# Performance work log

Hardware: AMD Instinct MI355X
Metric: run time of the kernel (lower is better)

Reference implementation:

```python
import jax, jax.numpy as jnp
import numpy as np

T_MAX = 20  # max_seq_length


def setup_inputs() -> dict:
    key = jax.random.key(0)
    ks = jax.random.split(key, 24)
    B, H, A, V, Tc = 64, 512, 512, 50257, 19
    s = 0.02
    inp = {}
    inp["features"] = jax.random.normal(ks[0], (B, H), jnp.float32)
    inp["captions"] = jax.random.randint(ks[1], (B, Tc), 0, V)
    lens = jax.random.randint(ks[2], (B, 1), 1, T_MAX + 1)
    inp["lengths"] = -jnp.sort(-lens, axis=0)  # descending so sort_ind is identity
    inp["embed_table"] = jax.random.uniform(ks[3], (V, H), jnp.float32, -0.1, 0.1)
    # LSTM cell (PyTorch layout): input = [emb; attended] -> 2H
    inp["W_ih"] = jax.random.normal(ks[4], (4 * H, 2 * H), jnp.float32) * s
    inp["W_hh"] = jax.random.normal(ks[5], (4 * H, H), jnp.float32) * s
    inp["b_ih"] = jnp.zeros((4 * H,), jnp.float32)
    inp["b_hh"] = jnp.zeros((4 * H,), jnp.float32)
    # attention
    inp["W_enc"] = jax.random.normal(ks[6], (H, A), jnp.float32) * s
    inp["b_enc"] = jnp.zeros((A,), jnp.float32)
    inp["W_dec"] = jax.random.normal(ks[7], (H, A), jnp.float32) * s
    inp["b_dec"] = jnp.zeros((A,), jnp.float32)
    inp["W_full"] = jax.random.normal(ks[8], (A, 1), jnp.float32) * s
    inp["b_full"] = jnp.zeros((1,), jnp.float32)
    # init_h / init_c / f_beta / fc
    inp["W_hinit"] = jax.random.normal(ks[9], (H, H), jnp.float32) * s
    inp["b_hinit"] = jnp.zeros((H,), jnp.float32)
    inp["W_cinit"] = jax.random.normal(ks[10], (H, H), jnp.float32) * s
    inp["b_cinit"] = jnp.zeros((H,), jnp.float32)
    inp["W_beta"] = jax.random.normal(ks[11], (H, H), jnp.float32) * s
    inp["b_beta"] = jnp.zeros((H,), jnp.float32)
    inp["W_fc"] = jax.random.uniform(ks[12], (H, V), jnp.float32, -0.1, 0.1)
    inp["b_fc"] = jnp.zeros((V,), jnp.float32)
    return inp


def _decode(features, embed_table, W_ih, W_hh, b_ih, b_hh, W_enc, b_enc,
            W_dec, b_dec, W_full, b_full, W_hinit, b_hinit, W_cinit, b_cinit,
            W_beta, b_beta, W_fc, b_fc, captions, lengths):
    B, H = features.shape
    emb = embed_table[captions]                               # (B, T-1, H)
    embeddings = jnp.concatenate([features[:, None, :], emb], axis=1)  # (B, T, H)
    encoder_out = features[:, None, :]                        # (B, 1, H) num_pixels=1
    mean_enc = encoder_out.mean(axis=1)
    h0 = mean_enc @ W_hinit + b_hinit
    c0 = mean_enc @ W_cinit + b_cinit
    att1 = encoder_out @ W_enc + b_enc                        # (B, 1, A), time-invariant
    lens = lengths[:, 0]

    def step(carry, xs):
        h, c = carry
        emb_t, t = xs
        # attention
        att2 = h @ W_dec + b_dec                              # (B, A)
        e = jax.nn.relu(att1 + att2[:, None, :]) @ W_full + b_full  # (B, 1, 1)
        alpha = jax.nn.softmax(e[..., 0], axis=1)             # (B, 1)
        awe = (encoder_out * alpha[..., None]).sum(axis=1)    # (B, H)
        gate = jax.nn.sigmoid(h @ W_beta + b_beta)
        awe = gate * awe
        # LSTM cell (PyTorch gate order i, f, g, o)
        x = jnp.concatenate([emb_t, awe], axis=1)             # (B, 2H)
        gates = x @ W_ih.T + b_ih + h @ W_hh.T + b_hh
        i, f, g, o = jnp.split(gates, 4, axis=1)
        c_new = jax.nn.sigmoid(f) * c + jax.nn.sigmoid(i) * jnp.tanh(g)
        h_new = jax.nn.sigmoid(o) * jnp.tanh(c_new)
        preds = h_new @ W_fc + b_fc                           # (B, V)
        mask = (t < lens)[:, None]
        h = jnp.where(mask, h_new, h)
        c = jnp.where(mask, c_new, c)
        out_t = jnp.where(mask, preds, jnp.zeros_like(preds))
        return (h, c), out_t

    xs = (embeddings.transpose(1, 0, 2), jnp.arange(T_MAX))
    _, outs = jax.lax.scan(step, (h0, c0), xs)                # (T, B, V)
    return outs.transpose(1, 0, 2)                            # (B, T, V)


def reference(features, captions, lengths, embed_table, W_ih, W_hh, b_ih, b_hh,
              W_enc, b_enc, W_dec, b_dec, W_full, b_full, W_hinit, b_hinit,
              W_cinit, b_cinit, W_beta, b_beta, W_fc, b_fc):
    return _decode(features, embed_table, W_ih, W_hh, b_ih, b_hh, W_enc, b_enc,
                   W_dec, b_dec, W_full, b_full, W_hinit, b_hinit, W_cinit,
                   b_cinit, W_beta, b_beta, W_fc, b_fc, captions, lengths)
```

## Files before the change

kernel.cpp:

```cpp
#include <hip/hip_runtime.h>
#include <hip/hip_bf16.h>


#define VV 50257
#define VP 50304
#define TT 20
#define NWRK 32
#define NTILES 6288
#define NNT 393
#define NGJOBS (TT*NNT)

typedef __attribute__((ext_vector_type(4))) float f32x4;
typedef __attribute__((ext_vector_type(8))) short bf16x8;

#define MFMA(a,b,c) __builtin_amdgcn_mfma_f32_16x16x32_bf16((a),(b),(c),0,0,0)

__device__ __forceinline__ unsigned short f2bf(float f){
  union { float f; unsigned int u; } v; v.f = f;
  unsigned int u = v.u;
  return (unsigned short)((u + 0x7FFFu + ((u >> 16) & 1u)) >> 16);
}
__device__ __forceinline__ float sigf(float x){ return 1.f/(1.f + expf(-x)); }

__device__ __forceinline__ void gload_lds16(const unsigned short* g, unsigned short* l){
  __builtin_amdgcn_global_load_lds(
      (const __attribute__((address_space(1))) unsigned int*)g,
      (__attribute__((address_space(3))) unsigned int*)l, 16, 0, 0);
}

__device__ __forceinline__ void l2_load16(bf16x8* d, const unsigned short* p){
  asm volatile("global_load_dwordx4 %0, %1, off sc0" : "=v"(*d) : "v"(p));
}
__device__ __forceinline__ void l2_store2(unsigned short* p, unsigned short v){
  asm volatile("global_store_short %0, %1, off sc0" :: "v"(p), "v"(v) : "memory");
}
__device__ __forceinline__ void llc_store2(unsigned short* p, unsigned short v){
  asm volatile("global_store_short %0, %1, off sc0 sc1" :: "v"(p), "v"(v) : "memory");
}
__device__ __forceinline__ unsigned int llc_load_u32(const unsigned int* p){
  unsigned int r;
  asm volatile("global_load_dword %0, %1, off sc0 sc1\n\ts_waitcnt vmcnt(0)"
               : "=v"(r) : "v"(p) : "memory");
  return r;
}

__device__ __forceinline__ void gbar(unsigned int* flags, int widx, unsigned target){
  asm volatile("s_waitcnt vmcnt(0)" ::: "memory");
  __syncthreads();
  if(threadIdx.x == 0){
    asm volatile("global_store_dword %0, %1, off sc0 sc1"
                 :: "v"(flags + widx), "v"(target) : "memory");
  }
  if(threadIdx.x < 64){
    const unsigned int* p = flags + (threadIdx.x & 31);
    for(;;){
      unsigned v = llc_load_u32(p);
      if(__all((int)(v >= target))) break;
      __builtin_amdgcn_s_sleep(1);
    }
  }
  __syncthreads();
}

__global__ __launch_bounds__(256) void prep(const float* __restrict__ Wih,
    const float* __restrict__ Whh, unsigned short* __restrict__ Wcomb,
    unsigned short* __restrict__ We,
    const float* __restrict__ Wbeta, unsigned short* __restrict__ Wbt,
    const float* __restrict__ feat, const float* __restrict__ emb,
    const int* __restrict__ cap, unsigned short* __restrict__ EmbMat,
    const float* __restrict__ Whi, const float* __restrict__ bhi,
    const float* __restrict__ Wci, const float* __restrict__ bci,
    unsigned short* __restrict__ xbuf, float* __restrict__ cbuf){
  __shared__ float tile[64][65];
  const int blk = blockIdx.x, tid = threadIdx.x;
  if(blk < 2048){
    int j = blk;
    for(int q=0;q<4;q++){ int k = tid + 256*q;
      float v = (k < 512) ? Whh[j*512 + k] : Wih[j*1024 + k];
      Wcomb[(size_t)j*1024 + k] = f2bf(v); }
    for(int q=0;q<2;q++){ int k = tid + 256*q;
      We[(size_t)j*512 + k] = f2bf(Wih[j*1024 + k]); }
  } else if(blk < 2112){
    int tb = blk - 2048;
    int c0 = (tb & 7)*64, r0 = (tb >> 3)*64;
    int tx = tid & 63, ty = tid >> 6;
    for(int i=0;i<16;i++){
      int r = ty + i*4;
      tile[r][tx] = Wbeta[(size_t)(r0+r)*512 + c0 + tx];
    }
    __syncthreads();
    for(int i=0;i<16;i++){
      int cl = ty + i*4;
      Wbt[(size_t)(c0+cl)*512 + r0 + tx] = f2bf(tile[tx][cl]);
    }
  } else if(blk < 3392){
    int m = blk - 2112; int t = m >> 6, b = m & 63;
    const float* src = (t == 0) ? (feat + b*512) : (emb + (size_t)cap[b*19 + (t-1)]*512);
    for(int q=0;q<2;q++){ int k = tid + 256*q;
      EmbMat[(size_t)m*512 + k] = f2bf(src[k]); }
  } else {
    int b = blk - 3392;
    float ah0 = bhi[tid], ah1 = bhi[tid+256];
    float ac0 = bci[tid], ac1 = bci[tid+256];
    for(int k=0;k<512;k++){
      float f = feat[b*512 + k];
      ah0 += f * Whi[k*512 + tid];     ah1 += f * Whi[k*512 + tid + 256];
      ac0 += f * Wci[k*512 + tid];     ac1 += f * Wci[k*512 + tid + 256];
    }
    xbuf[b*512 + tid] = f2bf(ah0);  xbuf[b*512 + tid + 256] = f2bf(ah1);
    cbuf[b*512 + tid] = ac0;        cbuf[b*512 + tid + 256] = ac1;
  }
}

__global__ __launch_bounds__(256) void gemmE(const unsigned short* __restrict__ Abf,
    const unsigned short* __restrict__ Bbf, const float* __restrict__ bias1,
    const float* __restrict__ bias2, float* __restrict__ Cout, int MT){
  __shared__ __align__(16) unsigned short As[128*64];
  __shared__ __align__(16) unsigned short Bs[128*64];
  const int nwg = gridDim.x;
  const int id = blockIdx.x;
  const int q = nwg >> 3, rr = nwg & 7;
  const int xcd = id & 7, pos = id >> 3;
  const int work = (xcd < rr) ? (xcd*(q+1) + pos) : (rr*(q+1) + (xcd-rr)*q + pos);
  const int m0 = (work % MT) * 128;
  const int n0 = (work / MT) * 128;
  const int tid = threadIdx.x, lane = tid & 63, w = tid >> 6;
  const int wr = w >> 1, wc = w & 1;
  const int lrow = lane >> 3, lcol = (lane & 7) * 8;
  const int l15 = lane & 15, lhi = lane >> 4;

  f32x4 acc[4][4];
#pragma unroll
  for(int i=0;i<4;i++)
#pragma unroll
    for(int j=0;j<4;j++) acc[i][j] = f32x4{0.f,0.f,0.f,0.f};

  for(int k0=0;k0<512;k0+=64){
    __syncthreads();
#pragma unroll
    for(int i=0;i<4;i++){
      int c = w*4 + i;
      int row = c*8 + lrow;
      gload_lds16(Abf + (size_t)(m0+row)*512 + k0 + lcol, As + c*512);
      gload_lds16(Bbf + (size_t)(n0+row)*512 + k0 + lcol, Bs + c*512);
    }
    asm volatile("s_waitcnt vmcnt(0)" ::: "memory");
    __syncthreads();
#pragma unroll
    for(int kk=0;kk<64;kk+=32){
      bf16x8 af[4], bfv[4];
#pragma unroll
      for(int mf=0;mf<4;mf++)
        af[mf] = *(const bf16x8*)(As + (wr*64 + mf*16 + l15)*64 + kk + lhi*8);
#pragma unroll
      for(int nf=0;nf<4;nf++)
        bfv[nf] = *(const bf16x8*)(Bs + (wc*64 + nf*16 + l15)*64 + kk + lhi*8);
#pragma unroll
      for(int mf=0;mf<4;mf++)
#pragma unroll
        for(int nf=0;nf<4;nf++)
          acc[mf][nf] = MFMA(af[mf], bfv[nf], acc[mf][nf]);
    }
  }
#pragma unroll
  for(int mf=0;mf<4;mf++)
#pragma unroll
    for(int nf=0;nf<4;nf++){
      int n = n0 + wc*64 + nf*16 + l15;
#pragma unroll
      for(int r=0;r<4;r++){
        int m = m0 + wr*64 + mf*16 + lhi*4 + r;
        int gate = n >> 9, col = n & 511;
        Cout[((size_t)m*512 + col)*4 + gate] = acc[mf][nf][r] + bias1[n] + bias2[n];
      }
    }
}

__global__ __launch_bounds__(256) void recur(
    const unsigned short* __restrict__ Wcomb,
    const unsigned short* __restrict__ Wbt,
    const float* __restrict__ bbeta,
    const float* __restrict__ feat,
    const float* __restrict__ E4,
    const float* __restrict__ c0,
    const int* __restrict__ lens,
    unsigned short* xbuf,
    unsigned short* awbuf,
    unsigned short* hs,
    unsigned int* ctrs,
    const float* __restrict__ Wfc, unsigned short* Wfct,
    const float* __restrict__ bfc, float* __restrict__ out){
  extern __shared__ char LDS[];
  int* lsh = (int*)LDS;
  const int tid = threadIdx.x;

  if(tid == 0){
    unsigned xcc = 99;
    asm volatile("s_getreg_b32 %0, hwreg(HW_REG_XCC_ID)" : "=s"(xcc));
    unsigned my = 0xffffffffu;
    if(xcc == 0) my = atomicAdd(&ctrs[0], 1u);
    lsh[0] = (my < NWRK) ? 1 : 0;
    lsh[1] = (int)my;
  }
  __syncthreads();
  const int iswork = lsh[0];
  const int widx = lsh[1];
  unsigned int* flags = &ctrs[32];
  __syncthreads();

  if(!iswork){
    const int lane = tid & 63, w = tid >> 6;
    const int lrow = lane >> 3, lcol = (lane & 7)*8;
    const int l15 = lane & 15, lhi = lane >> 4;
    unsigned short* As = (unsigned short*)LDS;
    unsigned short* Bs = (unsigned short*)(LDS + 8192);
    float* et = (float*)LDS;
    float (*tile)[65] = (float(*)[65])LDS;
    int* tk = (int*)(LDS + 147440);
    bool tdone = false;

    for(;;){
      __syncthreads();
      if(tid == 0) *tk = (int)atomicAdd(&ctrs[1], 1u);
      __syncthreads();
      int j = *tk;
      __syncthreads();
      if(j >= NTILES + NGJOBS) return;

      if(j < NTILES){
        int c0t = (j % 786)*64, r0 = (j / 786)*64;
        int tx = tid & 63, ty = tid >> 6;
        for(int i=0;i<16;i++){
          int r = ty + i*4; int sc = c0t + tx;
          tile[r][tx] = (sc < VV) ? Wfc[(size_t)(r0+r)*VV + sc] : 0.f;
        }
        __syncthreads();
        for(int i=0;i<16;i++){
          int cl = ty + i*4;
          llc_store2(Wfct + (size_t)(c0t+cl)*512 + r0 + tx, f2bf(tile[tx][cl]));
        }
        asm volatile("s_waitcnt vmcnt(0)" ::: "memory");
        __syncthreads();
        if(tid == 0) atomicAdd(&ctrs[2], 1u);
        continue;
      }

      int g = j - NTILES;
      int t = g / NNT, nt = g % NNT;
      int n0 = nt * 128;
      if(!tdone){
        if(tid == 0){
          while(llc_load_u32(&ctrs[2]) < NTILES) __builtin_amdgcn_s_sleep(8);
        }
        __syncthreads();
        tdone = true;
      }
      if(tid < 64){
        const unsigned int* p = flags + (tid & 31);
        unsigned tgt = (unsigned)(2*t + 2);
        for(;;){
          unsigned v = llc_load_u32(p);
          if(__all((int)(v >= tgt))) break;
          __builtin_amdgcn_s_sleep(4);
        }
      }
      __syncthreads();

      f32x4 acc[4][2];
#pragma unroll
      for(int i=0;i<4;i++){ acc[i][0] = f32x4{0.f,0.f,0.f,0.f};
                            acc[i][1] = f32x4{0.f,0.f,0.f,0.f}; }
      for(int k0=0;k0<512;k0+=64){
        __syncthreads();
        if(w < 2){
#pragma unroll
          for(int i=0;i<4;i++){
            int c = w*4 + i; int row = c*8 + lrow;
            gload_lds16(hs + (size_t)(t*64 + row)*512 + k0 + lcol, As + c*512);
          }
        }
#pragma unroll
        for(int i=0;i<4;i++){
          int c = w*4 + i; int row = c*8 + lrow;
          gload_lds16(Wfct + (size_t)(n0 + row)*512 + k0 + lcol, Bs + c*512);
        }
        asm volatile("s_waitcnt vmcnt(0)" ::: "memory");
        __syncthreads();
#pragma unroll
        for(int kk=0;kk<64;kk+=32){
          bf16x8 af[4], bv[2];
#pragma unroll
          for(int mf=0;mf<4;mf++)
            af[mf] = *(const bf16x8*)(As + (mf*16 + l15)*64 + kk + lhi*8);
#pragma unroll
          for(int nf=0;nf<2;nf++)
            bv[nf] = *(const bf16x8*)(Bs + (w*32 + nf*16 + l15)*64 + kk + lhi*8);
#pragma unroll
          for(int mf=0;mf<4;mf++){
            acc[mf][0] = MFMA(af[mf], bv[0], acc[mf][0]);
            acc[mf][1] = MFMA(af[mf], bv[1], acc[mf][1]);
          }
        }
      }
      __syncthreads();
      float bias[2];
#pragma unroll
      for(int nf=0;nf<2;nf++){
        int n = n0 + w*32 + nf*16 + l15;
        bias[nf] = (n < VV) ? bfc[n] : 0.f;
      }
#pragma unroll
      for(int mf=0;mf<4;mf++){
#pragma unroll
        for(int r=0;r<4;r++){
          int row = mf*16 + lhi*4 + r;
          bool valid = t < lens[row];
#pragma unroll
          for(int nf=0;nf<2;nf++){
            float v = valid ? (acc[mf][nf][r] + bias[nf]) : 0.f;
            et[row*128 + w*32 + nf*16 + l15] = v;
          }
        }
      }
      __syncthreads();
      const bool edge = (n0 + 128 > VV);
#pragma unroll
      for(int qq=0;qq<8;qq++){
        int idx = tid + 256*qq;
        int row = idx >> 5, c4 = idx & 31;
        const float* er = et + row*128;
        size_t bdw = (size_t)(row*20 + t)*VV + n0;
        if(!edge){
          int al = (int)((4 - (bdw & 3)) & 3);
          int chunks = (128 - al) >> 2;
          int tail = (128 - al) & 3;
          if(c4 < chunks){
            int s0 = al + c4*4;
            f32x4 v; v[0]=er[s0]; v[1]=er[s0+1]; v[2]=er[s0+2]; v[3]=er[s0+3];
            *(f32x4*)(out + bdw + s0) = v;
          }
          if(c4 < al) out[bdw + c4] = er[c4];
          if(c4 < tail){ int s1 = al + chunks*4 + c4; out[bdw + s1] = er[s1]; }
        } else {
#pragma unroll
          for(int i=0;i<4;i++){
            int cg = n0 + c4*4 + i;
            if(cg < VV) out[bdw + (c4*4 + i)] = er[c4*4 + i];
          }
        }
      }
    }
  }

  char* WCb = LDS;
  char* WBb = LDS + 131072;
  const int lane = tid & 63, w = tid >> 6;
  const int l15 = lane & 15, lhi = lane >> 4;
  const int jj0 = widx * 16;
  const int jj = jj0 + l15;
  const int arow = w*16 + l15;

  for(int cid = tid; cid < 8192; cid += 256){
    int gr = cid >> 7, cc = cid & 127;
    size_t gg = (size_t)(gr >> 4)*512 + jj0 + (gr & 15);
    bf16x8 v = *(const bf16x8*)(Wcomb + gg*1024 + cc*8);
    *(bf16x8*)(WCb + gr*2048 + ((cc*16) ^ ((gr & 7) << 4))) = v;
  }
  for(int cid = tid; cid < 1024; cid += 256){
    int r = cid >> 6, cc = cid & 63;
    bf16x8 v = *(const bf16x8*)(Wbt + (size_t)(jj0 + r)*512 + cc*8);
    *(bf16x8*)(WBb + r*1024 + ((cc*16) ^ ((r & 7) << 4))) = v;
  }

  float c_reg[4], fe[4]; int ln[4]; unsigned short hold[4];
#pragma unroll
  for(int r=0;r<4;r++){
    int b = w*16 + lhi*4 + r;
    c_reg[r] = c0[b*512 + jj];
    fe[r]    = feat[b*512 + jj];
    ln[r]    = lens[b];
    hold[r]  = xbuf[b*512 + jj];
  }
  const float bb = bbeta[jj];
  const unsigned short* pAx = xbuf  + (size_t)arow*512 + lhi*8;
  const unsigned short* pAw = awbuf + (size_t)arow*512 + lhi*8;
  __syncthreads();

  for(int t=0;t<TT;t++){
    bf16x8 a[16];
#pragma unroll
    for(int i=0;i<16;i++) l2_load16(&a[i], pAx + i*32);
    asm volatile("s_waitcnt vmcnt(0)" ::: "memory");
    __builtin_amdgcn_sched_barrier(0);

    f32x4 acca = f32x4{0.f,0.f,0.f,0.f};
    f32x4 accg[4];
#pragma unroll
    for(int i=0;i<4;i++) accg[i] = f32x4{0.f,0.f,0.f,0.f};
#pragma unroll
    for(int i=0;i<16;i++){
      int kb2 = i*64 + lhi*16;
      bf16x8 wb = *(const bf16x8*)(WBb + l15*1024 + (kb2 ^ ((l15 & 7) << 4)));
      acca = MFMA(a[i], wb, acca);
#pragma unroll
      for(int nf=0; nf<4; nf++){
        int gr = nf*16 + l15;
        bf16x8 wg = *(const bf16x8*)(WCb + gr*2048 + (kb2 ^ ((gr & 7) << 4)));
        accg[nf] = MFMA(a[i], wg, accg[nf]);
      }
    }
#pragma unroll
    for(int r=0;r<4;r++){
      int b = w*16 + lhi*4 + r;
      float g = sigf(acca[r] + bb);
      l2_store2(awbuf + b*512 + jj, f2bf(g * fe[r]));
    }
    gbar(flags, widx, (unsigned)(2*t+1));

    f32x4 e4v[4];
#pragma unroll
    for(int r=0;r<4;r++){
      int b = w*16 + lhi*4 + r;
      e4v[r] = *(const f32x4*)(E4 + (((size_t)(t*64 + b))*512 + jj)*4);
    }
#pragma unroll
    for(int i=0;i<16;i++) l2_load16(&a[i], pAw + i*32);
    asm volatile("s_waitcnt vmcnt(0)" ::: "memory");
    __builtin_amdgcn_sched_barrier(0);
#pragma unroll
    for(int i=0;i<16;i++){
      int kb2 = 1024 + i*64 + lhi*16;
#pragma unroll
      for(int nf=0; nf<4; nf++){
        int gr = nf*16 + l15;
        bf16x8 wg = *(const bf16x8*)(WCb + gr*2048 + (kb2 ^ ((gr & 7) << 4)));
        accg[nf] = MFMA(a[i], wg, accg[nf]);
      }
    }

#pragma unroll
    for(int r=0;r<4;r++){
      int b = w*16 + lhi*4 + r;
      float iv = sigf(accg[0][r] + e4v[r][0]);
      float fv = sigf(accg[1][r] + e4v[r][1]);
      float gv = tanhf(accg[2][r] + e4v[r][2]);
      float ov = sigf(accg[3][r] + e4v[r][3]);
      float cn = fv*c_reg[r] + iv*gv;
      float hn = ov * tanhf(cn);
      bool valid = t < ln[r];
      if(valid) c_reg[r] = cn;
      unsigned short hb = valid ? f2bf(hn) : hold[r];
      hold[r] = hb;
      llc_store2(hs + (size_t)(t*64 + b)*512 + jj, hb);
      l2_store2(xbuf + b*512 + jj, hb);
    }
    gbar(flags, widx, (unsigned)(2*t+2));
  }
}

extern "C" void kernel_launch(void* const* d_in, const int* in_sizes, int n_in,
                              void* d_out, int out_size, void* d_ws, size_t ws_size,
                              hipStream_t stream){
  const float* feat  = (const float*)d_in[0];
  const int*   cap   = (const int*)  d_in[1];
  const int*   lens  = (const int*)  d_in[2];
  const float* emb   = (const float*)d_in[3];
  const float* Wih   = (const float*)d_in[4];
  const float* Whh   = (const float*)d_in[5];
  const float* bih   = (const float*)d_in[6];
  const float* bhh   = (const float*)d_in[7];
  const float* Whi   = (const float*)d_in[14];
  const float* bhi   = (const float*)d_in[15];
  const float* Wci   = (const float*)d_in[16];
  const float* bci   = (const float*)d_in[17];
  const float* Wbeta = (const float*)d_in[18];
  const float* bbeta = (const float*)d_in[19];
  const float* Wfc   = (const float*)d_in[20];
  const float* bfc   = (const float*)d_in[21];
  float* out = (float*)d_out;

  char* ws = (char*)d_ws;
  size_t off = 0;
  auto alloc = [&](size_t bytes)->void*{
    void* p = ws + off; off += (bytes + 1023) & ~(size_t)1023; return p; };
  unsigned short* Wcomb  = (unsigned short*)alloc((size_t)2048*1024*2);
  unsigned short* We     = (unsigned short*)alloc((size_t)2048*512*2);
  unsigned short* Wbt    = (unsigned short*)alloc((size_t)512*512*2);
  unsigned short* Wfct   = (unsigned short*)alloc((size_t)VP*512*2);
  unsigned short* EmbMat = (unsigned short*)alloc((size_t)1280*512*2);
  float*          E4     = (float*)alloc((size_t)1280*2048*4);
  unsigned short* xbuf   = (unsigned short*)alloc((size_t)64*512*2);
  unsigned short* awbuf  = (unsigned short*)alloc((size_t)64*512*2);
  float*          cbuf   = (float*)alloc((size_t)64*512*4);
  unsigned short* hs     = (unsigned short*)alloc((size_t)1280*512*2);
  unsigned int*   ctrs   = (unsigned int*)alloc(256);

  static_cast<void>(hipFuncSetAttribute((const void*)recur,
      hipFuncAttributeMaxDynamicSharedMemorySize, 147456));

  hipMemsetAsync(ctrs, 0, 256, stream);

  prep<<<3456, 256, 0, stream>>>(Wih, Whh, Wcomb, We, Wbeta, Wbt, feat, emb,
                                 cap, EmbMat, Whi, bhi, Wci, bci, xbuf, cbuf);

  gemmE<<<160, 256, 0, stream>>>(EmbMat, We, bih, bhh, E4, 10);

  recur<<<256, 256, 147456, stream>>>(Wcomb, Wbt, bbeta, feat, E4, cbuf, lens,
                                      xbuf, awbuf, hs, ctrs, Wfc, Wfct, bfc, out);
}
```

Measured before the change: 660.5 us.

## Keep vocab weight tile resident in LDS across all timesteps in output GEMM

```diff
diff --git a/kernel.cpp b/kernel.cpp
--- a/kernel.cpp
+++ b/kernel.cpp
@@ -8,7 +8,6 @@
 #define NWRK 32
 #define NTILES 6288
 #define NNT 393
-#define NGJOBS (TT*NNT)
 
 typedef __attribute__((ext_vector_type(4))) float f32x4;
 typedef __attribute__((ext_vector_type(8))) short bf16x8;
@@ -28,33 +27,34 @@
       (__attribute__((address_space(3))) unsigned int*)l, 16, 0, 0);
 }
 
-__device__ __forceinline__ void l2_load16(bf16x8* d, const unsigned short* p){
-  asm volatile("global_load_dwordx4 %0, %1, off sc0" : "=v"(*d) : "v"(p));
-}
-__device__ __forceinline__ void l2_store2(unsigned short* p, unsigned short v){
-  asm volatile("global_store_short %0, %1, off sc0" :: "v"(p), "v"(v) : "memory");
-}
-__device__ __forceinline__ void llc_store2(unsigned short* p, unsigned short v){
+__device__ __forceinline__ void co_load16(bf16x8* d, const unsigned short* p){
+  asm volatile("global_load_dwordx4 %0, %1, off sc0 sc1" : "=v"(*d) : "v"(p));
+}
+__device__ __forceinline__ void co_store2(unsigned short* p, unsigned short v){
   asm volatile("global_store_short %0, %1, off sc0 sc1" :: "v"(p), "v"(v) : "memory");
 }
-__device__ __forceinline__ unsigned int llc_load_u32(const unsigned int* p){
+__device__ __forceinline__ unsigned int co_load_u32(const unsigned int* p){
   unsigned int r;
   asm volatile("global_load_dword %0, %1, off sc0 sc1\n\ts_waitcnt vmcnt(0)"
                : "=v"(r) : "v"(p) : "memory");
   return r;
 }
-
-__device__ __forceinline__ void gbar(unsigned int* flags, int widx, unsigned target){
+__device__ __forceinline__ void co_store_u32(unsigned int* p, unsigned int v){
+  asm volatile("global_store_dword %0, %1, off sc0 sc1" :: "v"(p), "v"(v) : "memory");
+}
+
+__device__ __forceinline__ void gbar(unsigned int* wflags, unsigned int* pflags,
+                                     int widx, unsigned target){
   asm volatile("s_waitcnt vmcnt(0)" ::: "memory");
   __syncthreads();
   if(threadIdx.x == 0){
-    asm volatile("global_store_dword %0, %1, off sc0 sc1"
-                 :: "v"(flags + widx), "v"(target) : "memory");
+    co_store_u32(pflags + widx, target);
+    co_store_u32(wflags + widx, target);
   }
   if(threadIdx.x < 64){
-    const unsigned int* p = flags + (threadIdx.x & 31);
+    const unsigned int* p = wflags + (threadIdx.x & 31);
     for(;;){
-      unsigned v = llc_load_u32(p);
+      unsigned v = co_load_u32(p);
       if(__all((int)(v >= target))) break;
       __builtin_amdgcn_s_sleep(1);
     }
@@ -205,19 +205,22 @@
   __syncthreads();
   const int iswork = lsh[0];
   const int widx = lsh[1];
-  unsigned int* flags = &ctrs[32];
+  unsigned int* wflags = &ctrs[32];
+  unsigned int* pflags = &ctrs[64];
   __syncthreads();
 
   if(!iswork){
     const int lane = tid & 63, w = tid >> 6;
-    const int lrow = lane >> 3, lcol = (lane & 7)*8;
     const int l15 = lane & 15, lhi = lane >> 4;
-    unsigned short* As = (unsigned short*)LDS;
-    unsigned short* Bs = (unsigned short*)(LDS + 8192);
-    float* et = (float*)LDS;
+    unsigned short* Bs = (unsigned short*)LDS;
+    float* et = (float*)(LDS + 131072);
     float (*tile)[65] = (float(*)[65])LDS;
-    int* tk = (int*)(LDS + 147440);
+    int* tk = (int*)(LDS + 147456);
     bool tdone = false;
+
+    int lnv[4];
+#pragma unroll
+    for(int r=0;r<4;r++) lnv[r] = lens[w*16 + lhi*4 + r];
 
     for(;;){
       __syncthreads();
@@ -225,7 +228,7 @@
       __syncthreads();
       int j = *tk;
       __syncthreads();
-      if(j >= NTILES + NGJOBS) return;
+      if(j >= NTILES + NNT) return;
 
       if(j < NTILES){
         int c0t = (j % 786)*64, r0 = (j / 786)*64;
@@ -237,7 +240,7 @@
         __syncthreads();
         for(int i=0;i<16;i++){
           int cl = ty + i*4;
-          llc_store2(Wfct + (size_t)(c0t+cl)*512 + r0 + tx, f2bf(tile[tx][cl]));
+          co_store2(Wfct + (size_t)(c0t+cl)*512 + r0 + tx, f2bf(tile[tx][cl]));
         }
         asm volatile("s_waitcnt vmcnt(0)" ::: "memory");
         __syncthreads();
@@ -245,107 +248,100 @@
         continue;
       }
 
-      int g = j - NTILES;
-      int t = g / NNT, nt = g % NNT;
-      int n0 = nt * 128;
       if(!tdone){
         if(tid == 0){
-          while(llc_load_u32(&ctrs[2]) < NTILES) __builtin_amdgcn_s_sleep(8);
+          while(co_load_u32(&ctrs[2]) < NTILES) __builtin_amdgcn_s_sleep(16);
         }
         __syncthreads();
         tdone = true;
       }
-      if(tid < 64){
-        const unsigned int* p = flags + (tid & 31);
-        unsigned tgt = (unsigned)(2*t + 2);
-        for(;;){
-          unsigned v = llc_load_u32(p);
-          if(__all((int)(v >= tgt))) break;
-          __builtin_amdgcn_s_sleep(4);
-        }
+      const int nt = j - NTILES;
+      const int n0 = nt * 128;
+#pragma unroll
+      for(int i=0;i<32;i++){
+        int cid = tid + 256*i;
+        int row = cid >> 6, cc = cid & 63;
+        bf16x8 v = *(const bf16x8*)(Wfct + (size_t)(n0 + row)*512 + cc*8);
+        *(bf16x8*)((char*)Bs + row*1024 + ((cc*16) ^ ((row & 7) << 4))) = v;
+      }
+      float bias[8];
+#pragma unroll
+      for(int nf=0;nf<8;nf++){
+        int n = n0 + nf*16 + l15;
+        bias[nf] = (n < VV) ? bfc[n] : 0.f;
       }
       __syncthreads();
-
-      f32x4 acc[4][2];
-#pragma unroll
-      for(int i=0;i<4;i++){ acc[i][0] = f32x4{0.f,0.f,0.f,0.f};
-                            acc[i][1] = f32x4{0.f,0.f,0.f,0.f}; }
-      for(int k0=0;k0<512;k0+=64){
-        __syncthreads();
-        if(w < 2){
-#pragma unroll
-          for(int i=0;i<4;i++){
-            int c = w*4 + i; int row = c*8 + lrow;
-            gload_lds16(hs + (size_t)(t*64 + row)*512 + k0 + lcol, As + c*512);
+      const bool edge = (n0 + 128 > VV);
+
+      for(int t=0;t<TT;t++){
+        if(tid < 64){
+          const unsigned int* p = pflags + (tid & 31);
+          unsigned tgt = (unsigned)(2*t + 2);
+          for(;;){
+            unsigned v = co_load_u32(p);
+            if(__all((int)(v >= tgt))) break;
+            __builtin_amdgcn_s_sleep(8);
           }
         }
-#pragma unroll
-        for(int i=0;i<4;i++){
-          int c = w*4 + i; int row = c*8 + lrow;
-          gload_lds16(Wfct + (size_t)(n0 + row)*512 + k0 + lcol, Bs + c*512);
-        }
+        __syncthreads();
+        bf16x8 af[16];
+        const unsigned short* pA = hs + (size_t)(t*64 + w*16 + l15)*512 + lhi*8;
+#pragma unroll
+        for(int i=0;i<16;i++) co_load16(&af[i], pA + i*32);
         asm volatile("s_waitcnt vmcnt(0)" ::: "memory");
-        __syncthreads();
-#pragma unroll
-        for(int kk=0;kk<64;kk+=32){
-          bf16x8 af[4], bv[2];
-#pragma unroll
-          for(int mf=0;mf<4;mf++)
-            af[mf] = *(const bf16x8*)(As + (mf*16 + l15)*64 + kk + lhi*8);
-#pragma unroll
-          for(int nf=0;nf<2;nf++)
-            bv[nf] = *(const bf16x8*)(Bs + (w*32 + nf*16 + l15)*64 + kk + lhi*8);
-#pragma unroll
-          for(int mf=0;mf<4;mf++){
-            acc[mf][0] = MFMA(af[mf], bv[0], acc[mf][0]);
-            acc[mf][1] = MFMA(af[mf], bv[1], acc[mf][1]);
+        __builtin_amdgcn_sched_barrier(0);
+        f32x4 acc[8];
+#pragma unroll
+        for(int nf=0;nf<8;nf++) acc[nf] = f32x4{0.f,0.f,0.f,0.f};
+#pragma unroll
+        for(int i=0;i<16;i++){
+          int kb2 = i*64 + lhi*16;
+#pragma unroll
+          for(int nf=0;nf<8;nf++){
+            int gr = nf*16 + l15;
+            bf16x8 bv = *(const bf16x8*)((char*)Bs + gr*1024 + (kb2 ^ ((gr & 7) << 4)));
+            acc[nf] = MFMA(af[i], bv, acc[nf]);
           }
         }
-      }
-      __syncthreads();
-      float bias[2];
-#pragma unroll
-      for(int nf=0;nf<2;nf++){
-        int n = n0 + w*32 + nf*16 + l15;
-        bias[nf] = (n < VV) ? bfc[n] : 0.f;
-      }
-#pragma unroll
-      for(int mf=0;mf<4;mf++){
-#pragma unroll
-        for(int r=0;r<4;r++){
-          int row = mf*16 + lhi*4 + r;
-          bool valid = t < lens[row];
-#pragma unroll
-          for(int nf=0;nf<2;nf++){
-            float v = valid ? (acc[mf][nf][r] + bias[nf]) : 0.f;
-            et[row*128 + w*32 + nf*16 + l15] = v;
+        for(int h=0; h<2; h++){
+          __syncthreads();
+          if((w >> 1) == h){
+#pragma unroll
+            for(int nf=0;nf<8;nf++){
+#pragma unroll
+              for(int r=0;r<4;r++){
+                bool valid = t < lnv[r];
+                float v = valid ? (acc[nf][r] + bias[nf]) : 0.f;
+                et[((w & 1)*16 + lhi*4 + r)*128 + nf*16 + l15] = v;
+              }
+            }
           }
-        }
-      }
-      __syncthreads();
-      const bool edge = (n0 + 128 > VV);
-#pragma unroll
-      for(int qq=0;qq<8;qq++){
-        int idx = tid + 256*qq;
-        int row = idx >> 5, c4 = idx & 31;
-        const float* er = et + row*128;
-        size_t bdw = (size_t)(row*20 + t)*VV + n0;
-        if(!edge){
-          int al = (int)((4 - (bdw & 3)) & 3);
-          int chunks = (128 - al) >> 2;
-          int tail = (128 - al) & 3;
-          if(c4 < chunks){
-            int s0 = al + c4*4;
-            f32x4 v; v[0]=er[s0]; v[1]=er[s0+1]; v[2]=er[s0+2]; v[3]=er[s0+3];
-            *(f32x4*)(out + bdw + s0) = v;
-          }
-          if(c4 < al) out[bdw + c4] = er[c4];
-          if(c4 < tail){ int s1 = al + chunks*4 + c4; out[bdw + s1] = er[s1]; }
-        } else {
-#pragma unroll
-          for(int i=0;i<4;i++){
-            int cg = n0 + c4*4 + i;
-            if(cg < VV) out[bdw + (c4*4 + i)] = er[c4*4 + i];
+          __syncthreads();
+#pragma unroll
+          for(int qq=0;qq<4;qq++){
+            int idx = tid + 256*qq;
+            int rowl = idx >> 5, c4 = idx & 31;
+            int b = h*32 + rowl;
+            const float* er = et + rowl*128;
+            size_t bdw = (size_t)(b*20 + t)*VV + n0;
+            if(!edge){
+              int al = (int)((4 - (bdw & 3)) & 3);
+              int chunks = (128 - al) >> 2;
+              int tail = (128 - al) & 3;
+              if(c4 < chunks){
+                int s0 = al + c4*4;
+                f32x4 v; v[0]=er[s0]; v[1]=er[s0+1]; v[2]=er[s0+2]; v[3]=er[s0+3];
+                *(f32x4*)(out + bdw + s0) = v;
+              }
+              if(c4 < al) out[bdw + c4] = er[c4];
+              if(c4 < tail){ int s1 = al + chunks*4 + c4; out[bdw + s1] = er[s1]; }
+            } else {
+#pragma unroll
+              for(int i2=0;i2<4;i2++){
+                int cg = n0 + c4*4 + i2;
+                if(cg < VV) out[bdw + (c4*4 + i2)] = er[c4*4 + i2];
+              }
+            }
           }
         }
       }
@@ -387,9 +383,15 @@
   __syncthreads();
 
   for(int t=0;t<TT;t++){
+    f32x4 e4v[4];
+#pragma unroll
+    for(int r=0;r<4;r++){
+      int b = w*16 + lhi*4 + r;
+      e4v[r] = *(const f32x4*)(E4 + (((size_t)(t*64 + b))*512 + jj)*4);
+    }
     bf16x8 a[16];
 #pragma unroll
-    for(int i=0;i<16;i++) l2_load16(&a[i], pAx + i*32);
+    for(int i=0;i<16;i++) co_load16(&a[i], pAx + i*32);
     asm volatile("s_waitcnt vmcnt(0)" ::: "memory");
     __builtin_amdgcn_sched_barrier(0);
 
@@ -413,18 +415,12 @@
     for(int r=0;r<4;r++){
       int b = w*16 + lhi*4 + r;
       float g = sigf(acca[r] + bb);
-      l2_store2(awbuf + b*512 + jj, f2bf(g * fe[r]));
-    }
-    gbar(flags, widx, (unsigned)(2*t+1));
-
-    f32x4 e4v[4];
-#pragma unroll
-    for(int r=0;r<4;r++){
-      int b = w*16 + lhi*4 + r;
-      e4v[r] = *(const f32x4*)(E4 + (((size_t)(t*64 + b))*512 + jj)*4);
-    }
-#pragma unroll
-    for(int i=0;i<16;i++) l2_load16(&a[i], pAw + i*32);
+      co_store2(awbuf + b*512 + jj, f2bf(g * fe[r]));
+    }
+    gbar(wflags, pflags, widx, (unsigned)(2*t+1));
+
+#pragma unroll
+    for(int i=0;i<16;i++) co_load16(&a[i], pAw + i*32);
     asm volatile("s_waitcnt vmcnt(0)" ::: "memory");
     __builtin_amdgcn_sched_barrier(0);
 #pragma unroll
@@ -451,10 +447,10 @@
       if(valid) c_reg[r] = cn;
       unsigned short hb = valid ? f2bf(hn) : hold[r];
       hold[r] = hb;
-      llc_store2(hs + (size_t)(t*64 + b)*512 + jj, hb);
-      l2_store2(xbuf + b*512 + jj, hb);
-    }
-    gbar(flags, widx, (unsigned)(2*t+2));
+      co_store2(hs + (size_t)(t*64 + b)*512 + jj, hb);
+      co_store2(xbuf + b*512 + jj, hb);
+    }
+    gbar(wflags, pflags, widx, (unsigned)(2*t+2));
   }
 }
 
@@ -493,18 +489,18 @@
   unsigned short* awbuf  = (unsigned short*)alloc((size_t)64*512*2);
   float*          cbuf   = (float*)alloc((size_t)64*512*4);
   unsigned short* hs     = (unsigned short*)alloc((size_t)1280*512*2);
-  unsigned int*   ctrs   = (unsigned int*)alloc(256);
+  unsigned int*   ctrs   = (unsigned int*)alloc(512);
 
   static_cast<void>(hipFuncSetAttribute((const void*)recur,
-      hipFuncAttributeMaxDynamicSharedMemorySize, 147456));
-
-  hipMemsetAsync(ctrs, 0, 256, stream);
+      hipFuncAttributeMaxDynamicSharedMemorySize, 148480));
+
+  hipMemsetAsync(ctrs, 0, 512, stream);
 
   prep<<<3456, 256, 0, stream>>>(Wih, Whh, Wcomb, We, Wbeta, Wbt, feat, emb,
                                  cap, EmbMat, Whi, bhi, Wci, bci, xbuf, cbuf);
 
   gemmE<<<160, 256, 0, stream>>>(EmbMat, We, bih, bhh, E4, 10);
 
-  recur<<<256, 256, 147456, stream>>>(Wcomb, Wbt, bbeta, feat, E4, cbuf, lens,
+  recur<<<256, 256, 148480, stream>>>(Wcomb, Wbt, bbeta, feat, E4, cbuf, lens,
                                       xbuf, awbuf, hs, ctrs, Wfc, Wfct, bfc, out);
 }
```

New measurement: 622.8 us. 1.06x faster.
